# Kernel tuning notes

Hardware: AMD Instinct MI355X
Metric: run time of the kernel (lower is better)

Reference implementation:

```python
import jax, jax.numpy as jnp
import numpy as np

N_NODES = 50000
N_EDGES = 1600000
IN_CH = 128
OUT_CH = 64
N_HEADS = 4


def setup_inputs() -> dict:
    key = jax.random.key(0)
    k1, k2, k3, k4, k5 = jax.random.split(key, 5)
    x_source = jax.random.normal(k1, (N_NODES, IN_CH), dtype=jnp.float32)
    edge_tgt = jax.random.randint(k2, (N_EDGES,), 0, N_NODES, dtype=jnp.int32)
    edge_src = jax.random.randint(k3, (N_EDGES,), 0, N_NODES, dtype=jnp.int32)
    edge_vals = jnp.ones((N_EDGES,), dtype=jnp.float32)
    # per-head learned params (xavier_uniform-ish scale)
    w_scale = float(np.sqrt(6.0 / (IN_CH + OUT_CH)))
    weight = jax.random.uniform(k4, (N_HEADS, IN_CH, OUT_CH), dtype=jnp.float32,
                                minval=-w_scale, maxval=w_scale)
    a_scale = float(np.sqrt(6.0 / (2 * OUT_CH)))
    att_weight = jax.random.uniform(k5, (N_HEADS, 2 * OUT_CH), dtype=jnp.float32,
                                    minval=-a_scale, maxval=a_scale)
    return {"x_source": x_source, "edge_tgt": edge_tgt, "edge_src": edge_src,
            "edge_vals": edge_vals, "weight": weight, "att_weight": att_weight}


def _can_forward(x_source, edge_tgt, edge_src, edge_vals, weight, att_weight):
    n_nodes = x_source.shape[0]
    out_ch = weight.shape[-1]
    # per-head linear transform: [N, H, O]
    x_msg = jnp.einsum('ni,hio->nho', x_source, weight)
    # gather per-edge source/target messages: [E, H, O]
    src_msg = x_msg[edge_src]
    tgt_msg = x_msg[edge_tgt]
    # attention score = cat([src, tgt]) @ att_weight, split halves: [E, H]
    aw_s = att_weight[:, :out_ch]
    aw_t = att_weight[:, out_ch:]
    e = jnp.einsum('eho,ho->eh', src_msg, aw_s) + jnp.einsum('eho,ho->eh', tgt_msg, aw_t)
    e = jax.nn.leaky_relu(e, negative_slope=0.01)  # default torch slope
    e = e * edge_vals[:, None]  # multiply by neighborhood values pre-softmax
    # sparse softmax over each target row (dim=1 of the sparse matrix)
    row_max = jax.ops.segment_max(e, edge_tgt, num_segments=n_nodes)  # [N, H]
    e_exp = jnp.exp(e - row_max[edge_tgt])
    row_sum = jax.ops.segment_sum(e_exp, edge_tgt, num_segments=n_nodes)  # [N, H]
    alpha = e_exp / row_sum[edge_tgt]  # [E, H]
    # weighted aggregate of source messages per target node: [N, H, O]
    out = jax.ops.segment_sum(alpha[:, :, None] * src_msg, edge_tgt,
                              num_segments=n_nodes)
    # concat heads -> [N, H*O]
    return out.reshape(n_nodes, -1)


def reference(x_source, edge_tgt, edge_src, edge_vals, weight, att_weight):
    return _can_forward(x_source, edge_tgt, edge_src, edge_vals, weight, att_weight)
```

## Files before the change

kernel.cpp:

```cpp
#include <hip/hip_runtime.h>
#include <hip/hip_bf16.h>
#include <math.h>

#define N_NODES 50000
#define N_EDGES 1600000
#define IN_CH   128
#define OUT_CH  64
#define N_HEADS 4
#define CH      (N_HEADS * OUT_CH)

#define NPB   64
#define BINS  782
#define CAPB  3072
#define CHUNK 3200
#define NSCAT 500
#define GEMMB 782

typedef __attribute__((ext_vector_type(8))) short bf16x8;
typedef __attribute__((ext_vector_type(4))) float f32x4;

__device__ __forceinline__ float bf16_lo(unsigned u) { return __uint_as_float(u << 16); }
__device__ __forceinline__ float bf16_hi(unsigned u) { return __uint_as_float(u & 0xffff0000u); }
__device__ __forceinline__ unsigned short f_to_bf16(float f) {
  unsigned u = __float_as_uint(f);
  u += 0x7fffu + ((u >> 16) & 1u);
  return (unsigned short)(u >> 16);
}

__global__ __launch_bounds__(256) void convert_w_init(
    const float* __restrict__ w, unsigned short* __restrict__ wb, int* __restrict__ gcur)
{
  int i = blockIdx.x * 256 + threadIdx.x;
  if (i < BINS) gcur[i] = i * CAPB;
  if (i >= N_HEADS * IN_CH * OUT_CH) return;
  int j = i & 7, lane = (i >> 3) & 63, ctg = (i >> 9) & 15, kc = i >> 13;
  int k = kc * 32 + (lane >> 4) * 8 + j;
  int n = ctg * 16 + (lane & 15);
  int h = n >> 6, o = n & 63;
  wb[i] = f_to_bf16(w[(h * IN_CH + k) * OUT_CH + o]);
}

__global__ __launch_bounds__(256) void gemm_scatter(
    const float* __restrict__ x, const unsigned short* __restrict__ wb,
    const float* __restrict__ aw,
    unsigned short* __restrict__ xmsg, float* __restrict__ sbuf, float* __restrict__ tbuf,
    const int* __restrict__ etgt, const int* __restrict__ esrc,
    const float* __restrict__ eval, int* __restrict__ gcur, int2* __restrict__ binned)
{
  __shared__ __align__(16) char smem[32768];

  if (blockIdx.x < NSCAT) {
    int* lhist = (int*)smem;
    int* lbase = lhist + BINS;
    unsigned short* stg = (unsigned short*)(lbase + BINS);

    const int tid = threadIdx.x;
    const int e0 = blockIdx.x * CHUNK;
    const int n = min(CHUNK, N_EDGES - e0);

    for (int b = tid; b < BINS; b += 256) lhist[b] = 0;
    __syncthreads();

    for (int i = tid; i < n; i += 256) {
      int t = etgt[e0 + i];
      stg[i] = (unsigned short)t;
      atomicAdd(&lhist[t >> 6], 1);
    }
    __syncthreads();

    for (int b = tid; b < BINS; b += 256) {
      int c = lhist[b];
      lbase[b] = c ? atomicAdd(&gcur[b], c) : 0;
      lhist[b] = 0;
    }
    __syncthreads();

    for (int i = tid; i < n; i += 256) {
      int t = (int)stg[i];
      int b = t >> 6;
      int r = atomicAdd(&lhist[b], 1);
      int pos = lbase[b] + r;
      if (pos < (b + 1) * CAPB) {
        int pack = esrc[e0 + i] | ((t & 63) << 16);
        binned[pos] = make_int2(pack, __float_as_int(eval[e0 + i]));
      }
    }
    return;
  }

  unsigned short (*tlds)[32][128] = (unsigned short (*)[32][128])smem;

  const int gbid = blockIdx.x - NSCAT;
  const int lane = threadIdx.x & 63;
  const int wv   = threadIdx.x >> 6;
  const int q    = lane >> 4;
  const int l16  = lane & 15;
  const int rowbase = gbid * 64 + (wv >> 1) * 32;
  const int chalf   = wv & 1;

  bf16x8 afrag[2][4];
  #pragma unroll
  for (int s = 0; s < 2; ++s) {
    int r = rowbase + s * 16 + l16;
    r = min(r, N_NODES - 1);
    const float* xp = x + (size_t)r * IN_CH + q * 8;
    #pragma unroll
    for (int kc = 0; kc < 4; ++kc) {
      f32x4 lo = *(const f32x4*)(xp + kc * 32);
      f32x4 hi = *(const f32x4*)(xp + kc * 32 + 4);
      bf16x8 a;
      a[0] = (short)f_to_bf16(lo[0]); a[1] = (short)f_to_bf16(lo[1]);
      a[2] = (short)f_to_bf16(lo[2]); a[3] = (short)f_to_bf16(lo[3]);
      a[4] = (short)f_to_bf16(hi[0]); a[5] = (short)f_to_bf16(hi[1]);
      a[6] = (short)f_to_bf16(hi[2]); a[7] = (short)f_to_bf16(hi[3]);
      afrag[s][kc] = a;
    }
  }

  f32x4 acc[2][8];
  #pragma unroll
  for (int s = 0; s < 2; ++s)
    #pragma unroll
    for (int ct = 0; ct < 8; ++ct)
      acc[s][ct] = (f32x4){0.f, 0.f, 0.f, 0.f};

  #pragma unroll
  for (int kc = 0; kc < 4; ++kc) {
    #pragma unroll
    for (int ct = 0; ct < 8; ++ct) {
      const int ctg = chalf * 8 + ct;
      bf16x8 b = *(const bf16x8*)(wb + ((size_t)(kc * 16 + ctg) * 64 + lane) * 8);
      acc[0][ct] = __builtin_amdgcn_mfma_f32_16x16x32_bf16(afrag[0][kc], b, acc[0][ct], 0, 0, 0);
      acc[1][ct] = __builtin_amdgcn_mfma_f32_16x16x32_bf16(afrag[1][kc], b, acc[1][ct], 0, 0, 0);
    }
  }

  #pragma unroll
  for (int s = 0; s < 2; ++s)
    #pragma unroll
    for (int ct = 0; ct < 8; ++ct)
      #pragma unroll
      for (int reg = 0; reg < 4; ++reg)
        tlds[wv][s * 16 + q * 4 + reg][ct * 16 + l16] = f_to_bf16(acc[s][ct][reg]);

  #pragma unroll
  for (int s = 0; s < 2; ++s) {
    float ps[2][4] = {{0,0,0,0},{0,0,0,0}};
    float pt[2][4] = {{0,0,0,0},{0,0,0,0}};
    #pragma unroll
    for (int ct = 0; ct < 8; ++ct) {
      int col = chalf * 128 + ct * 16 + l16;
      int h = col >> 6;
      float as_ = aw[h * 128 + (col & 63)];
      float at_ = aw[h * 128 + 64 + (col & 63)];
      int hp = ct >> 2;
      #pragma unroll
      for (int reg = 0; reg < 4; ++reg) {
        float v = acc[s][ct][reg];
        ps[hp][reg] += v * as_;
        pt[hp][reg] += v * at_;
      }
    }
    #pragma unroll
    for (int hp = 0; hp < 2; ++hp)
      #pragma unroll
      for (int reg = 0; reg < 4; ++reg)
        #pragma unroll
        for (int off = 1; off < 16; off <<= 1) {
          ps[hp][reg] += __shfl_xor(ps[hp][reg], off);
          pt[hp][reg] += __shfl_xor(pt[hp][reg], off);
        }
    const int rowq = rowbase + s * 16 + q * 4;
    if (l16 == 0) {
      #pragma unroll
      for (int reg = 0; reg < 4; ++reg) {
        int r = rowq + reg;
        if (r < N_NODES) {
          #pragma unroll
          for (int hp = 0; hp < 2; ++hp) {
            sbuf[r * 4 + chalf * 2 + hp] = ps[hp][reg];
            tbuf[r * 4 + chalf * 2 + hp] = pt[hp][reg];
          }
        }
      }
    }
  }

  __syncthreads();

  const int seg  = lane & 31;
  const int half = lane >> 5;
  #pragma unroll
  for (int r2 = 0; r2 < 16; ++r2) {
    int row = r2 * 2 + half;
    int gr = rowbase + row;
    if (gr < N_NODES) {
      ushort4 vv = *(const ushort4*)&tlds[wv][row][seg * 4];
      *(ushort4*)(xmsg + (size_t)gr * CH + chalf * 128 + seg * 4) = vv;
    }
  }
}

__global__ __launch_bounds__(256) void build_csr(
    const int* __restrict__ gcur, const int2* __restrict__ binned,
    int2* __restrict__ csr, int* __restrict__ deg, int* __restrict__ rowstart)
{
  __shared__ int nh[NPB];
  __shared__ int npre[NPB];
  __shared__ __align__(16) int2 stg[CAPB];

  const int tid = threadIdx.x;
  const int b = blockIdx.x;
  const int base = b * CAPB;
  const int cnt = min(gcur[b] - base, CAPB);

  if (tid < NPB) nh[tid] = 0;
  __syncthreads();

  for (int i = tid; i < cnt; i += 256) {
    int2 e = binned[base + i];
    stg[i] = e;
    atomicAdd(&nh[(e.x >> 16) & 63], 1);
  }
  __syncthreads();

  if (tid < 64) {
    int v = nh[tid];
    int sc = v;
    #pragma unroll
    for (int off = 1; off < 64; off <<= 1) {
      int u = __shfl_up(sc, off);
      if (tid >= off) sc += u;
    }
    npre[tid] = sc - v;
    int node = b * NPB + tid;
    if (node < N_NODES) { deg[node] = v; rowstart[node] = base + sc - v; }
    nh[tid] = 0;
  }
  __syncthreads();

  for (int i = tid; i < cnt; i += 256) {
    int2 e = stg[i];
    int tl = (e.x >> 16) & 63;
    int r = atomicAdd(&nh[tl], 1);
    csr[base + npre[tl] + r] = e;
  }
}

__global__ __launch_bounds__(256) void aggregate_kernel(
    const int* __restrict__ deg, const int* __restrict__ rowstart,
    const int2* __restrict__ csr,
    const float* __restrict__ sbuf, const float* __restrict__ tbuf,
    const unsigned short* __restrict__ xmsg, float* __restrict__ out)
{
  const int lane = threadIdx.x & 63;
  const int wave = threadIdx.x >> 6;
  const int n = blockIdx.x * 4 + wave;
  if (n >= N_NODES) return;

  __shared__ __align__(16) float p_lds[4][64][4];
  __shared__ int s_lds[4][64];

  const int d = deg[n];
  const int rs0 = rowstart[n];
  const int seg  = lane & 31;
  const int half = lane >> 5;
  const int hh4  = seg >> 3;

  float4 tn4 = *(const float4*)(tbuf + (size_t)n * 4);
  float tn[4] = {tn4.x, tn4.y, tn4.z, tn4.w};

  float m[4]    = {-INFINITY, -INFINITY, -INFINITY, -INFINITY};
  float psum[4] = {0.f, 0.f, 0.f, 0.f};
  float acc[8]  = {0.f, 0.f, 0.f, 0.f, 0.f, 0.f, 0.f, 0.f};

  for (int base = 0; base < d; base += 64) {
    const int cnt = min(64, d - base);
    const bool act = lane < cnt;

    float sc[4] = {-INFINITY, -INFINITY, -INFINITY, -INFINITY};
    int s = 0;
    if (act) {
      int2 ev = csr[(size_t)rs0 + base + lane];
      s = ev.x & 0xffff;
      float v = __int_as_float(ev.y);
      float4 sv4 = *(const float4*)(sbuf + (size_t)s * 4);
      float svv[4] = {sv4.x, sv4.y, sv4.z, sv4.w};
      #pragma unroll
      for (int hh = 0; hh < 4; ++hh) {
        float t = svv[hh] + tn[hh];
        t = (t > 0.f) ? t : 0.01f * t;
        sc[hh] = t * v;
      }
    }

    float bm[4] = {sc[0], sc[1], sc[2], sc[3]};
    #pragma unroll
    for (int hh = 0; hh < 4; ++hh)
      #pragma unroll
      for (int off = 32; off; off >>= 1)
        bm[hh] = fmaxf(bm[hh], __shfl_xor(bm[hh], off));

    float p[4];
    #pragma unroll
    for (int hh = 0; hh < 4; ++hh) {
      float nm = fmaxf(m[hh], bm[hh]);
      float r = (m[hh] == -INFINITY) ? 0.f : __expf(m[hh] - nm);
      psum[hh] *= r;
      if (hh == hh4) {
        #pragma unroll
        for (int j = 0; j < 8; ++j) acc[j] *= r;
      }
      m[hh] = nm;
      p[hh] = act ? __expf(sc[hh] - nm) : 0.f;
      psum[hh] += p[hh];
    }

    if (act) {
      s_lds[wave][lane] = s;
      *(float4*)(&p_lds[wave][lane][0]) = make_float4(p[0], p[1], p[2], p[3]);
    }
    __builtin_amdgcn_wave_barrier();

    int k = 0;
    for (; k + 8 <= cnt; k += 8) {
      int sA = s_lds[wave][k + 0 + half];
      int sB = s_lds[wave][k + 2 + half];
      int sC = s_lds[wave][k + 4 + half];
      int sD = s_lds[wave][k + 6 + half];
      uint4 rA = *(const uint4*)(xmsg + (size_t)sA * CH + seg * 8);
      uint4 rB = *(const uint4*)(xmsg + (size_t)sB * CH + seg * 8);
      uint4 rC = *(const uint4*)(xmsg + (size_t)sC * CH + seg * 8);
      uint4 rD = *(const uint4*)(xmsg + (size_t)sD * CH + seg * 8);
      float qA = p_lds[wave][k + 0 + half][hh4];
      float qB = p_lds[wave][k + 2 + half][hh4];
      float qC = p_lds[wave][k + 4 + half][hh4];
      float qD = p_lds[wave][k + 6 + half][hh4];
      acc[0] = fmaf(qA, bf16_lo(rA.x), acc[0]); acc[1] = fmaf(qA, bf16_hi(rA.x), acc[1]);
      acc[2] = fmaf(qA, bf16_lo(rA.y), acc[2]); acc[3] = fmaf(qA, bf16_hi(rA.y), acc[3]);
      acc[4] = fmaf(qA, bf16_lo(rA.z), acc[4]); acc[5] = fmaf(qA, bf16_hi(rA.z), acc[5]);
      acc[6] = fmaf(qA, bf16_lo(rA.w), acc[6]); acc[7] = fmaf(qA, bf16_hi(rA.w), acc[7]);
      acc[0] = fmaf(qB, bf16_lo(rB.x), acc[0]); acc[1] = fmaf(qB, bf16_hi(rB.x), acc[1]);
      acc[2] = fmaf(qB, bf16_lo(rB.y), acc[2]); acc[3] = fmaf(qB, bf16_hi(rB.y), acc[3]);
      acc[4] = fmaf(qB, bf16_lo(rB.z), acc[4]); acc[5] = fmaf(qB, bf16_hi(rB.z), acc[5]);
      acc[6] = fmaf(qB, bf16_lo(rB.w), acc[6]); acc[7] = fmaf(qB, bf16_hi(rB.w), acc[7]);
      acc[0] = fmaf(qC, bf16_lo(rC.x), acc[0]); acc[1] = fmaf(qC, bf16_hi(rC.x), acc[1]);
      acc[2] = fmaf(qC, bf16_lo(rC.y), acc[2]); acc[3] = fmaf(qC, bf16_hi(rC.y), acc[3]);
      acc[4] = fmaf(qC, bf16_lo(rC.z), acc[4]); acc[5] = fmaf(qC, bf16_hi(rC.z), acc[5]);
      acc[6] = fmaf(qC, bf16_lo(rC.w), acc[6]); acc[7] = fmaf(qC, bf16_hi(rC.w), acc[7]);
      acc[0] = fmaf(qD, bf16_lo(rD.x), acc[0]); acc[1] = fmaf(qD, bf16_hi(rD.x), acc[1]);
      acc[2] = fmaf(qD, bf16_lo(rD.y), acc[2]); acc[3] = fmaf(qD, bf16_hi(rD.y), acc[3]);
      acc[4] = fmaf(qD, bf16_lo(rD.z), acc[4]); acc[5] = fmaf(qD, bf16_hi(rD.z), acc[5]);
      acc[6] = fmaf(qD, bf16_lo(rD.w), acc[6]); acc[7] = fmaf(qD, bf16_hi(rD.w), acc[7]);
    }
    for (; k < cnt; k += 2) {
      int e = k + half;
      if (e < cnt) {
        int sA = s_lds[wave][e];
        uint4 rA = *(const uint4*)(xmsg + (size_t)sA * CH + seg * 8);
        float qA = p_lds[wave][e][hh4];
        acc[0] = fmaf(qA, bf16_lo(rA.x), acc[0]); acc[1] = fmaf(qA, bf16_hi(rA.x), acc[1]);
        acc[2] = fmaf(qA, bf16_lo(rA.y), acc[2]); acc[3] = fmaf(qA, bf16_hi(rA.y), acc[3]);
        acc[4] = fmaf(qA, bf16_lo(rA.z), acc[4]); acc[5] = fmaf(qA, bf16_hi(rA.z), acc[5]);
        acc[6] = fmaf(qA, bf16_lo(rA.w), acc[6]); acc[7] = fmaf(qA, bf16_hi(rA.w), acc[7]);
      }
    }
    __builtin_amdgcn_wave_barrier();
  }

  #pragma unroll
  for (int j = 0; j < 8; ++j) acc[j] += __shfl_xor(acc[j], 32);
  #pragma unroll
  for (int hh = 0; hh < 4; ++hh)
    #pragma unroll
    for (int off = 32; off; off >>= 1)
      psum[hh] += __shfl_xor(psum[hh], off);

  float rs = psum[hh4];
  float inv = (rs > 0.f) ? 1.0f / rs : 0.f;
  const int o = half * 4;
  float4 o4 = make_float4(acc[o+0]*inv, acc[o+1]*inv, acc[o+2]*inv, acc[o+3]*inv);
  *(float4*)(out + (size_t)n * CH + seg * 8 + half * 4) = o4;
}

extern "C" void kernel_launch(void* const* d_in, const int* in_sizes, int n_in,
                              void* d_out, int out_size, void* d_ws, size_t ws_size,
                              hipStream_t stream) {
  const float* x    = (const float*)d_in[0];
  const int*   etgt = (const int*)  d_in[1];
  const int*   esrc = (const int*)  d_in[2];
  const float* evl  = (const float*)d_in[3];
  const float* w    = (const float*)d_in[4];
  const float* aw   = (const float*)d_in[5];
  float* out = (float*)d_out;

  char* ws = (char*)d_ws;
  unsigned short* wb   = (unsigned short*)(ws);
  unsigned short* xmsg = (unsigned short*)(ws + 65536);
  float* sbuf     = (float*)(ws + 25665536);
  float* tbuf     = (float*)(ws + 26465536);
  int*   gcur     = (int*)  (ws + 27265536);
  int*   deg      = (int*)  (ws + 27269632);
  int*   rowstart = (int*)  (ws + 27470336);
  int2*  binned   = (int2*) (ws + 27671040);
  int2*  csr      = (int2*) (ws + 46889472);

  convert_w_init<<<128, 256, 0, stream>>>(w, wb, gcur);
  gemm_scatter<<<NSCAT + GEMMB, 256, 0, stream>>>(x, wb, aw, xmsg, sbuf, tbuf,
                                                  etgt, esrc, evl, gcur, binned);
  build_csr<<<BINS, 256, 0, stream>>>(gcur, binned, csr, deg, rowstart);
  aggregate_kernel<<<(N_NODES + 3) / 4, 256, 0, stream>>>(deg, rowstart, csr,
                                                          sbuf, tbuf, xmsg, out);
}
```

Measured before the change: 276.4 us.

## Build CSR with global atomic count-scan-scatter and use half-wave per node aggregation

Replaces the two-pass LDS-binned CSR construction with a simpler pipeline. Per-node degrees are counted with global atomics alongside the GEMM, then a per-bin wave scan produces row starts, and edges are scattered into the CSR through per-node atomic cursors. The aggregation kernel now gives each 32-lane half-wave its own target node, with 16 nodes per block, to cut idle lanes at the average degree of about 32. The trade-off is millions of contended global atomics and random 8-byte writes in place of LDS-local atomics and coalesced bin writes. Each half-wave also loops to the larger of the two paired nodes' degrees.

Result: slower. 420.2 us (+52.0%).

```diff
diff --git a/kernel.cpp b/kernel.cpp
--- a/kernel.cpp
+++ b/kernel.cpp
@@ -12,9 +12,10 @@
 #define NPB   64
 #define BINS  782
 #define CAPB  3072
-#define CHUNK 3200
-#define NSCAT 500
+#define NCNT  256
 #define GEMMB 782
+#define NSCAT 512
+#define NPBLK 16
 
 typedef __attribute__((ext_vector_type(8))) short bf16x8;
 typedef __attribute__((ext_vector_type(4))) float f32x4;
@@ -28,10 +29,10 @@
 }
 
 __global__ __launch_bounds__(256) void convert_w_init(
-    const float* __restrict__ w, unsigned short* __restrict__ wb, int* __restrict__ gcur)
+    const float* __restrict__ w, unsigned short* __restrict__ wb, int* __restrict__ deg)
 {
   int i = blockIdx.x * 256 + threadIdx.x;
-  if (i < BINS) gcur[i] = i * CAPB;
+  if (i < N_NODES) deg[i] = 0;
   if (i >= N_HEADS * IN_CH * OUT_CH) return;
   int j = i & 7, lane = (i >> 3) & 63, ctg = (i >> 9) & 15, kc = i >> 13;
   int k = kc * 32 + (lane >> 4) * 8 + j;
@@ -40,57 +41,22 @@
   wb[i] = f_to_bf16(w[(h * IN_CH + k) * OUT_CH + o]);
 }
 
-__global__ __launch_bounds__(256) void gemm_scatter(
+__global__ __launch_bounds__(256) void gemm_count(
     const float* __restrict__ x, const unsigned short* __restrict__ wb,
     const float* __restrict__ aw,
     unsigned short* __restrict__ xmsg, float* __restrict__ sbuf, float* __restrict__ tbuf,
-    const int* __restrict__ etgt, const int* __restrict__ esrc,
-    const float* __restrict__ eval, int* __restrict__ gcur, int2* __restrict__ binned)
-{
-  __shared__ __align__(16) char smem[32768];
-
-  if (blockIdx.x < NSCAT) {
-    int* lhist = (int*)smem;
-    int* lbase = lhist + BINS;
-    unsigned short* stg = (unsigned short*)(lbase + BINS);
-
-    const int tid = threadIdx.x;
-    const int e0 = blockIdx.x * CHUNK;
-    const int n = min(CHUNK, N_EDGES - e0);
-
-    for (int b = tid; b < BINS; b += 256) lhist[b] = 0;
-    __syncthreads();
-
-    for (int i = tid; i < n; i += 256) {
-      int t = etgt[e0 + i];
-      stg[i] = (unsigned short)t;
-      atomicAdd(&lhist[t >> 6], 1);
-    }
-    __syncthreads();
-
-    for (int b = tid; b < BINS; b += 256) {
-      int c = lhist[b];
-      lbase[b] = c ? atomicAdd(&gcur[b], c) : 0;
-      lhist[b] = 0;
-    }
-    __syncthreads();
-
-    for (int i = tid; i < n; i += 256) {
-      int t = (int)stg[i];
-      int b = t >> 6;
-      int r = atomicAdd(&lhist[b], 1);
-      int pos = lbase[b] + r;
-      if (pos < (b + 1) * CAPB) {
-        int pack = esrc[e0 + i] | ((t & 63) << 16);
-        binned[pos] = make_int2(pack, __float_as_int(eval[e0 + i]));
-      }
-    }
+    const int* __restrict__ etgt, int* __restrict__ deg)
+{
+  __shared__ __align__(16) unsigned short tlds[4][32][128];
+
+  if (blockIdx.x < NCNT) {
+    const int stride = NCNT * 256;
+    for (int i = blockIdx.x * 256 + threadIdx.x; i < N_EDGES; i += stride)
+      atomicAdd(&deg[etgt[i]], 1);
     return;
   }
 
-  unsigned short (*tlds)[32][128] = (unsigned short (*)[32][128])smem;
-
-  const int gbid = blockIdx.x - NSCAT;
+  const int gbid = blockIdx.x - NCNT;
   const int lane = threadIdx.x & 63;
   const int wv   = threadIdx.x >> 6;
   const int q    = lane >> 4;
@@ -201,49 +167,34 @@
   }
 }
 
-__global__ __launch_bounds__(256) void build_csr(
-    const int* __restrict__ gcur, const int2* __restrict__ binned,
-    int2* __restrict__ csr, int* __restrict__ deg, int* __restrict__ rowstart)
-{
-  __shared__ int nh[NPB];
-  __shared__ int npre[NPB];
-  __shared__ __align__(16) int2 stg[CAPB];
-
-  const int tid = threadIdx.x;
-  const int b = blockIdx.x;
-  const int base = b * CAPB;
-  const int cnt = min(gcur[b] - base, CAPB);
-
-  if (tid < NPB) nh[tid] = 0;
-  __syncthreads();
-
-  for (int i = tid; i < cnt; i += 256) {
-    int2 e = binned[base + i];
-    stg[i] = e;
-    atomicAdd(&nh[(e.x >> 16) & 63], 1);
-  }
-  __syncthreads();
-
-  if (tid < 64) {
-    int v = nh[tid];
-    int sc = v;
-    #pragma unroll
-    for (int off = 1; off < 64; off <<= 1) {
-      int u = __shfl_up(sc, off);
-      if (tid >= off) sc += u;
-    }
-    npre[tid] = sc - v;
-    int node = b * NPB + tid;
-    if (node < N_NODES) { deg[node] = v; rowstart[node] = base + sc - v; }
-    nh[tid] = 0;
-  }
-  __syncthreads();
-
-  for (int i = tid; i < cnt; i += 256) {
-    int2 e = stg[i];
-    int tl = (e.x >> 16) & 63;
-    int r = atomicAdd(&nh[tl], 1);
-    csr[base + npre[tl] + r] = e;
+__global__ __launch_bounds__(256) void scan_bins(
+    const int* __restrict__ deg, int* __restrict__ rowstart, int* __restrict__ cursor)
+{
+  const int w = threadIdx.x >> 6;
+  const int lane = threadIdx.x & 63;
+  const int bin = blockIdx.x * 4 + w;
+  if (bin >= BINS) return;
+  const int node = bin * NPB + lane;
+  int v = (node < N_NODES) ? deg[node] : 0;
+  int sc = v;
+  #pragma unroll
+  for (int off = 1; off < 64; off <<= 1) {
+    int u = __shfl_up(sc, off);
+    if (lane >= off) sc += u;
+  }
+  int rs = bin * CAPB + sc - v;
+  if (node < N_NODES) { rowstart[node] = rs; cursor[node] = rs; }
+}
+
+__global__ __launch_bounds__(256) void scatter_csr(
+    const int* __restrict__ etgt, const int* __restrict__ esrc,
+    const float* __restrict__ eval, int* __restrict__ cursor, int2* __restrict__ csr)
+{
+  const int stride = NSCAT * 256;
+  for (int i = blockIdx.x * 256 + threadIdx.x; i < N_EDGES; i += stride) {
+    int t = etgt[i];
+    int pos = atomicAdd(&cursor[t], 1);
+    csr[pos] = make_int2(esrc[i], __float_as_int(eval[i]));
   }
 }
 
@@ -253,134 +204,123 @@
     const float* __restrict__ sbuf, const float* __restrict__ tbuf,
     const unsigned short* __restrict__ xmsg, float* __restrict__ out)
 {
-  const int lane = threadIdx.x & 63;
-  const int wave = threadIdx.x >> 6;
-  const int n = blockIdx.x * 4 + wave;
-  if (n >= N_NODES) return;
-
-  __shared__ __align__(16) float p_lds[4][64][4];
-  __shared__ int s_lds[4][64];
-
-  const int d = deg[n];
-  const int rs0 = rowstart[n];
-  const int seg  = lane & 31;
-  const int half = lane >> 5;
-  const int hh4  = seg >> 3;
-
-  float4 tn4 = *(const float4*)(tbuf + (size_t)n * 4);
-  float tn[4] = {tn4.x, tn4.y, tn4.z, tn4.w};
-
-  float m[4]    = {-INFINITY, -INFINITY, -INFINITY, -INFINITY};
-  float psum[4] = {0.f, 0.f, 0.f, 0.f};
-  float acc[8]  = {0.f, 0.f, 0.f, 0.f, 0.f, 0.f, 0.f, 0.f};
-
-  for (int base = 0; base < d; base += 64) {
-    const int cnt = min(64, d - base);
-    const bool act = lane < cnt;
-
-    float sc[4] = {-INFINITY, -INFINITY, -INFINITY, -INFINITY};
-    int s = 0;
-    if (act) {
-      int2 ev = csr[(size_t)rs0 + base + lane];
-      s = ev.x & 0xffff;
-      float v = __int_as_float(ev.y);
-      float4 sv4 = *(const float4*)(sbuf + (size_t)s * 4);
-      float svv[4] = {sv4.x, sv4.y, sv4.z, sv4.w};
+  __shared__ int s_lds[4][2][32];
+  __shared__ __align__(16) float p_lds[4][2][32][4];
+
+  const int tid  = threadIdx.x;
+  const int w    = tid >> 6;
+  const int lane = tid & 63;
+  const int hv   = lane >> 5;
+  const int l32  = lane & 31;
+  const int hh4  = l32 >> 3;
+
+  #pragma unroll
+  for (int it = 0; it < NPBLK / 8; ++it) {
+    const int n = blockIdx.x * NPBLK + it * 8 + w * 2 + hv;
+    const int d   = deg[n];
+    const int rs0 = rowstart[n];
+    const int dmax = max(d, __shfl_xor(d, 32));
+
+    float4 tn4 = *(const float4*)(tbuf + (size_t)n * 4);
+    float tn[4] = {tn4.x, tn4.y, tn4.z, tn4.w};
+
+    float m[4]    = {-INFINITY, -INFINITY, -INFINITY, -INFINITY};
+    float psum[4] = {0.f, 0.f, 0.f, 0.f};
+    float acc[8]  = {0.f, 0.f, 0.f, 0.f, 0.f, 0.f, 0.f, 0.f};
+
+    for (int base = 0; base < dmax; base += 32) {
+      const int cnt = d - base;
+      const bool act = l32 < cnt;
+
+      float sc4[4] = {-INFINITY, -INFINITY, -INFINITY, -INFINITY};
+      int s = 0;
+      if (act) {
+        int2 ev = csr[(size_t)rs0 + base + l32];
+        s = ev.x;
+        float v = __int_as_float(ev.y);
+        float4 sv4 = *(const float4*)(sbuf + (size_t)s * 4);
+        float svv[4] = {sv4.x, sv4.y, sv4.z, sv4.w};
+        #pragma unroll
+        for (int hh = 0; hh < 4; ++hh) {
+          float t = svv[hh] + tn[hh];
+          t = (t > 0.f) ? t : 0.01f * t;
+          sc4[hh] = t * v;
+        }
+      }
+
+      float bm[4] = {sc4[0], sc4[1], sc4[2], sc4[3]};
+      #pragma unroll
+      for (int hh = 0; hh < 4; ++hh)
+        #pragma unroll
+        for (int off = 16; off; off >>= 1)
+          bm[hh] = fmaxf(bm[hh], __shfl_xor(bm[hh], off));
+
+      float p[4];
       #pragma unroll
       for (int hh = 0; hh < 4; ++hh) {
-        float t = svv[hh] + tn[hh];
-        t = (t > 0.f) ? t : 0.01f * t;
-        sc[hh] = t * v;
-      }
-    }
-
-    float bm[4] = {sc[0], sc[1], sc[2], sc[3]};
+        float nm = fmaxf(m[hh], bm[hh]);
+        float r = (m[hh] == -INFINITY) ? 0.f : __expf(m[hh] - nm);
+        psum[hh] *= r;
+        if (hh == hh4) {
+          #pragma unroll
+          for (int j = 0; j < 8; ++j) acc[j] *= r;
+        }
+        m[hh] = nm;
+        p[hh] = act ? __expf(sc4[hh] - nm) : 0.f;
+        psum[hh] += p[hh];
+      }
+
+      s_lds[w][hv][l32] = s;
+      *(float4*)(&p_lds[w][hv][l32][0]) = make_float4(p[0], p[1], p[2], p[3]);
+      __builtin_amdgcn_wave_barrier();
+
+      const int kmax = min(32, dmax - base);
+      for (int k = 0; k < kmax; k += 4) {
+        int s0 = s_lds[w][hv][k + 0];
+        int s1 = s_lds[w][hv][k + 1];
+        int s2 = s_lds[w][hv][k + 2];
+        int s3 = s_lds[w][hv][k + 3];
+        uint4 r0 = *(const uint4*)(xmsg + (size_t)s0 * CH + l32 * 8);
+        uint4 r1 = *(const uint4*)(xmsg + (size_t)s1 * CH + l32 * 8);
+        uint4 r2 = *(const uint4*)(xmsg + (size_t)s2 * CH + l32 * 8);
+        uint4 r3 = *(const uint4*)(xmsg + (size_t)s3 * CH + l32 * 8);
+        float q0 = p_lds[w][hv][k + 0][hh4];
+        float q1 = p_lds[w][hv][k + 1][hh4];
+        float q2 = p_lds[w][hv][k + 2][hh4];
+        float q3 = p_lds[w][hv][k + 3][hh4];
+        acc[0] = fmaf(q0, bf16_lo(r0.x), acc[0]); acc[1] = fmaf(q0, bf16_hi(r0.x), acc[1]);
+        acc[2] = fmaf(q0, bf16_lo(r0.y), acc[2]); acc[3] = fmaf(q0, bf16_hi(r0.y), acc[3]);
+        acc[4] = fmaf(q0, bf16_lo(r0.z), acc[4]); acc[5] = fmaf(q0, bf16_hi(r0.z), acc[5]);
+        acc[6] = fmaf(q0, bf16_lo(r0.w), acc[6]); acc[7] = fmaf(q0, bf16_hi(r0.w), acc[7]);
+        acc[0] = fmaf(q1, bf16_lo(r1.x), acc[0]); acc[1] = fmaf(q1, bf16_hi(r1.x), acc[1]);
+        acc[2] = fmaf(q1, bf16_lo(r1.y), acc[2]); acc[3] = fmaf(q1, bf16_hi(r1.y), acc[3]);
+        acc[4] = fmaf(q1, bf16_lo(r1.z), acc[4]); acc[5] = fmaf(q1, bf16_hi(r1.z), acc[5]);
+        acc[6] = fmaf(q1, bf16_lo(r1.w), acc[6]); acc[7] = fmaf(q1, bf16_hi(r1.w), acc[7]);
+        acc[0] = fmaf(q2, bf16_lo(r2.x), acc[0]); acc[1] = fmaf(q2, bf16_hi(r2.x), acc[1]);
+        acc[2] = fmaf(q2, bf16_lo(r2.y), acc[2]); acc[3] = fmaf(q2, bf16_hi(r2.y), acc[3]);
+        acc[4] = fmaf(q2, bf16_lo(r2.z), acc[4]); acc[5] = fmaf(q2, bf16_hi(r2.z), acc[5]);
+        acc[6] = fmaf(q2, bf16_lo(r2.w), acc[6]); acc[7] = fmaf(q2, bf16_hi(r2.w), acc[7]);
+        acc[0] = fmaf(q3, bf16_lo(r3.x), acc[0]); acc[1] = fmaf(q3, bf16_hi(r3.x), acc[1]);
+        acc[2] = fmaf(q3, bf16_lo(r3.y), acc[2]); acc[3] = fmaf(q3, bf16_hi(r3.y), acc[3]);
+        acc[4] = fmaf(q3, bf16_lo(r3.z), acc[4]); acc[5] = fmaf(q3, bf16_hi(r3.z), acc[5]);
+        acc[6] = fmaf(q3, bf16_lo(r3.w), acc[6]); acc[7] = fmaf(q3, bf16_hi(r3.w), acc[7]);
+      }
+      __builtin_amdgcn_wave_barrier();
+    }
+
     #pragma unroll
     for (int hh = 0; hh < 4; ++hh)
       #pragma unroll
-      for (int off = 32; off; off >>= 1)
-        bm[hh] = fmaxf(bm[hh], __shfl_xor(bm[hh], off));
-
-    float p[4];
-    #pragma unroll
-    for (int hh = 0; hh < 4; ++hh) {
-      float nm = fmaxf(m[hh], bm[hh]);
-      float r = (m[hh] == -INFINITY) ? 0.f : __expf(m[hh] - nm);
-      psum[hh] *= r;
-      if (hh == hh4) {
-        #pragma unroll
-        for (int j = 0; j < 8; ++j) acc[j] *= r;
-      }
-      m[hh] = nm;
-      p[hh] = act ? __expf(sc[hh] - nm) : 0.f;
-      psum[hh] += p[hh];
-    }
-
-    if (act) {
-      s_lds[wave][lane] = s;
-      *(float4*)(&p_lds[wave][lane][0]) = make_float4(p[0], p[1], p[2], p[3]);
-    }
-    __builtin_amdgcn_wave_barrier();
-
-    int k = 0;
-    for (; k + 8 <= cnt; k += 8) {
-      int sA = s_lds[wave][k + 0 + half];
-      int sB = s_lds[wave][k + 2 + half];
-      int sC = s_lds[wave][k + 4 + half];
-      int sD = s_lds[wave][k + 6 + half];
-      uint4 rA = *(const uint4*)(xmsg + (size_t)sA * CH + seg * 8);
-      uint4 rB = *(const uint4*)(xmsg + (size_t)sB * CH + seg * 8);
-      uint4 rC = *(const uint4*)(xmsg + (size_t)sC * CH + seg * 8);
-      uint4 rD = *(const uint4*)(xmsg + (size_t)sD * CH + seg * 8);
-      float qA = p_lds[wave][k + 0 + half][hh4];
-      float qB = p_lds[wave][k + 2 + half][hh4];
-      float qC = p_lds[wave][k + 4 + half][hh4];
-      float qD = p_lds[wave][k + 6 + half][hh4];
-      acc[0] = fmaf(qA, bf16_lo(rA.x), acc[0]); acc[1] = fmaf(qA, bf16_hi(rA.x), acc[1]);
-      acc[2] = fmaf(qA, bf16_lo(rA.y), acc[2]); acc[3] = fmaf(qA, bf16_hi(rA.y), acc[3]);
-      acc[4] = fmaf(qA, bf16_lo(rA.z), acc[4]); acc[5] = fmaf(qA, bf16_hi(rA.z), acc[5]);
-      acc[6] = fmaf(qA, bf16_lo(rA.w), acc[6]); acc[7] = fmaf(qA, bf16_hi(rA.w), acc[7]);
-      acc[0] = fmaf(qB, bf16_lo(rB.x), acc[0]); acc[1] = fmaf(qB, bf16_hi(rB.x), acc[1]);
-      acc[2] = fmaf(qB, bf16_lo(rB.y), acc[2]); acc[3] = fmaf(qB, bf16_hi(rB.y), acc[3]);
-      acc[4] = fmaf(qB, bf16_lo(rB.z), acc[4]); acc[5] = fmaf(qB, bf16_hi(rB.z), acc[5]);
-      acc[6] = fmaf(qB, bf16_lo(rB.w), acc[6]); acc[7] = fmaf(qB, bf16_hi(rB.w), acc[7]);
-      acc[0] = fmaf(qC, bf16_lo(rC.x), acc[0]); acc[1] = fmaf(qC, bf16_hi(rC.x), acc[1]);
-      acc[2] = fmaf(qC, bf16_lo(rC.y), acc[2]); acc[3] = fmaf(qC, bf16_hi(rC.y), acc[3]);
-      acc[4] = fmaf(qC, bf16_lo(rC.z), acc[4]); acc[5] = fmaf(qC, bf16_hi(rC.z), acc[5]);
-      acc[6] = fmaf(qC, bf16_lo(rC.w), acc[6]); acc[7] = fmaf(qC, bf16_hi(rC.w), acc[7]);
-      acc[0] = fmaf(qD, bf16_lo(rD.x), acc[0]); acc[1] = fmaf(qD, bf16_hi(rD.x), acc[1]);
-      acc[2] = fmaf(qD, bf16_lo(rD.y), acc[2]); acc[3] = fmaf(qD, bf16_hi(rD.y), acc[3]);
-      acc[4] = fmaf(qD, bf16_lo(rD.z), acc[4]); acc[5] = fmaf(qD, bf16_hi(rD.z), acc[5]);
-      acc[6] = fmaf(qD, bf16_lo(rD.w), acc[6]); acc[7] = fmaf(qD, bf16_hi(rD.w), acc[7]);
-    }
-    for (; k < cnt; k += 2) {
-      int e = k + half;
-      if (e < cnt) {
-        int sA = s_lds[wave][e];
-        uint4 rA = *(const uint4*)(xmsg + (size_t)sA * CH + seg * 8);
-        float qA = p_lds[wave][e][hh4];
-        acc[0] = fmaf(qA, bf16_lo(rA.x), acc[0]); acc[1] = fmaf(qA, bf16_hi(rA.x), acc[1]);
-        acc[2] = fmaf(qA, bf16_lo(rA.y), acc[2]); acc[3] = fmaf(qA, bf16_hi(rA.y), acc[3]);
-        acc[4] = fmaf(qA, bf16_lo(rA.z), acc[4]); acc[5] = fmaf(qA, bf16_hi(rA.z), acc[5]);
-        acc[6] = fmaf(qA, bf16_lo(rA.w), acc[6]); acc[7] = fmaf(qA, bf16_hi(rA.w), acc[7]);
-      }
-    }
-    __builtin_amdgcn_wave_barrier();
-  }
-
-  #pragma unroll
-  for (int j = 0; j < 8; ++j) acc[j] += __shfl_xor(acc[j], 32);
-  #pragma unroll
-  for (int hh = 0; hh < 4; ++hh)
-    #pragma unroll
-    for (int off = 32; off; off >>= 1)
-      psum[hh] += __shfl_xor(psum[hh], off);
-
-  float rs = psum[hh4];
-  float inv = (rs > 0.f) ? 1.0f / rs : 0.f;
-  const int o = half * 4;
-  float4 o4 = make_float4(acc[o+0]*inv, acc[o+1]*inv, acc[o+2]*inv, acc[o+3]*inv);
-  *(float4*)(out + (size_t)n * CH + seg * 8 + half * 4) = o4;
+      for (int off = 16; off; off >>= 1)
+        psum[hh] += __shfl_xor(psum[hh], off);
+
+    float rsum = psum[hh4];
+    float inv = (rsum > 0.f) ? 1.0f / rsum : 0.f;
+    float4 o0 = make_float4(acc[0] * inv, acc[1] * inv, acc[2] * inv, acc[3] * inv);
+    float4 o1 = make_float4(acc[4] * inv, acc[5] * inv, acc[6] * inv, acc[7] * inv);
+    *(float4*)(out + (size_t)n * CH + l32 * 8)     = o0;
+    *(float4*)(out + (size_t)n * CH + l32 * 8 + 4) = o1;
+  }
 }
 
 extern "C" void kernel_launch(void* const* d_in, const int* in_sizes, int n_in,
@@ -399,16 +339,15 @@
   unsigned short* xmsg = (unsigned short*)(ws + 65536);
   float* sbuf     = (float*)(ws + 25665536);
   float* tbuf     = (float*)(ws + 26465536);
-  int*   gcur     = (int*)  (ws + 27265536);
-  int*   deg      = (int*)  (ws + 27269632);
-  int*   rowstart = (int*)  (ws + 27470336);
-  int2*  binned   = (int2*) (ws + 27671040);
-  int2*  csr      = (int2*) (ws + 46889472);
-
-  convert_w_init<<<128, 256, 0, stream>>>(w, wb, gcur);
-  gemm_scatter<<<NSCAT + GEMMB, 256, 0, stream>>>(x, wb, aw, xmsg, sbuf, tbuf,
-                                                  etgt, esrc, evl, gcur, binned);
-  build_csr<<<BINS, 256, 0, stream>>>(gcur, binned, csr, deg, rowstart);
-  aggregate_kernel<<<(N_NODES + 3) / 4, 256, 0, stream>>>(deg, rowstart, csr,
-                                                          sbuf, tbuf, xmsg, out);
-}
+  int*   deg      = (int*)  (ws + 27265536);
+  int*   rowstart = (int*)  (ws + 27465536);
+  int*   cursor   = (int*)  (ws + 27665536);
+  int2*  csr      = (int2*) (ws + 27865536);
+
+  convert_w_init<<<256, 256, 0, stream>>>(w, wb, deg);
+  gemm_count<<<NCNT + GEMMB, 256, 0, stream>>>(x, wb, aw, xmsg, sbuf, tbuf, etgt, deg);
+  scan_bins<<<(BINS + 3) / 4, 256, 0, stream>>>(deg, rowstart, cursor);
+  scatter_csr<<<NSCAT, 256, 0, stream>>>(etgt, esrc, evl, cursor, csr);
+  aggregate_kernel<<<N_NODES / NPBLK, 256, 0, stream>>>(deg, rowstart, csr,
+                                                        sbuf, tbuf, xmsg, out);
+}
```
